# Kernel optimization log

Measured on AMD Instinct MI355X. Metric: run time of the kernel, lower is better.

The kernel has to match this reference:

```python
import jax, jax.numpy as jnp
import numpy as np

H = 16      # num_attention_heads
D = 1024    # hidden_size
DH = D // H # attention_head_size
LN_EPS = 1e-5


def setup_inputs() -> dict:
    key = jax.random.key(0)
    ks = jax.random.split(key, 12)
    B, S = 2, 2048
    s = 0.02
    return {
        "hidden_states": jax.random.normal(ks[0], (B, S, D), jnp.float32),
        "attention_mask": jnp.zeros((B, 1, 1, S), jnp.float32),
        "Wq": jax.random.normal(ks[1], (D, D), jnp.float32) * s,
        "bq": jnp.zeros((D,), jnp.float32),
        "Wk": jax.random.normal(ks[2], (D, D), jnp.float32) * s,
        "bk": jnp.zeros((D,), jnp.float32),
        "Wv": jax.random.normal(ks[3], (D, D), jnp.float32) * s,
        "bv": jnp.zeros((D,), jnp.float32),
        "med_bias": jax.random.normal(ks[4], (H, 1, 1), jnp.float32) * s,
        "Wo": jax.random.normal(ks[5], (D, D), jnp.float32) * s,
        "bo": jnp.zeros((D,), jnp.float32),
        "gamma": jnp.ones((D,), jnp.float32),
        "beta": jnp.zeros((D,), jnp.float32),
    }


def _heads(x):
    # (B,S,D) -> (B,H,S,DH)
    B, S, _ = x.shape
    return x.reshape(B, S, H, DH).transpose(0, 2, 1, 3)


def reference(hidden_states, attention_mask, Wq, bq, Wk, bk, Wv, bv,
              med_bias, Wo, bo, gamma, beta):
    B, S, _ = hidden_states.shape
    q = _heads(hidden_states @ Wq.T + bq)
    k = _heads(hidden_states @ Wk.T + bk)
    v = _heads(hidden_states @ Wv.T + bv)

    scale = 1.0 / jnp.sqrt(jnp.asarray(DH, hidden_states.dtype))
    # scores: (B,H,S,S); per-head medical bias + additive mask
    scores = jnp.einsum('bhqd,bhkd->bhqk', q, k) * scale
    scores = scores + med_bias[None, :, :, :] + attention_mask
    probs = jax.nn.softmax(scores, axis=-1)  # dropout is identity in eval

    ctx = jnp.einsum('bhqk,bhkd->bhqd', probs, v)
    ctx = ctx.transpose(0, 2, 1, 3).reshape(B, S, D)

    attn_out = ctx @ Wo.T + bo
    x = hidden_states + attn_out

    mu = jnp.mean(x, axis=-1, keepdims=True)
    var = jnp.mean(jnp.square(x - mu), axis=-1, keepdims=True)
    return (x - mu) * jax.lax.rsqrt(var + LN_EPS) * gamma + beta
```

## Files before the change

### kernel.cpp

```cpp
#include <hip/hip_runtime.h>
#include <hip/hip_bf16.h>

#define S_LEN 2048
#define NH 16
#define DH 64
#define DMODEL 1024
#define M_TOT 4096
#define LOG2E 1.44269504f

typedef __attribute__((ext_vector_type(8))) short bf16x8;
typedef __attribute__((ext_vector_type(4))) float f32x4;
typedef unsigned short u16;
typedef unsigned short us8 __attribute__((ext_vector_type(8)));

__device__ inline u16 f2bf(float f) {
    union { float f; unsigned u; } c; c.f = f;
    unsigned r = c.u + 0x7fffu + ((c.u >> 16) & 1u);
    return (u16)(r >> 16);
}

__device__ inline void load_lds16(const u16* g, u16* l) {
    __builtin_amdgcn_global_load_lds((const __attribute__((address_space(1))) void*)g,
                                     (__attribute__((address_space(3))) void*)l, 16, 0, 0);
}

__device__ inline us8 pack8(float4 a, float4 b) {
    us8 o;
    o[0] = f2bf(a.x); o[1] = f2bf(a.y); o[2] = f2bf(a.z); o[3] = f2bf(a.w);
    o[4] = f2bf(b.x); o[5] = f2bf(b.y); o[6] = f2bf(b.z); o[7] = f2bf(b.w);
    return o;
}

__global__ __launch_bounds__(256) void conv_bf16(
    const float* __restrict__ src, u16* __restrict__ dst)
{
    const size_t i = ((size_t)blockIdx.x * 256 + threadIdx.x) * 8;
    const float4 a = *(const float4*)(src + i);
    const float4 b = *(const float4*)(src + i + 4);
    *(us8*)(dst + i) = pack8(a, b);
}

__global__ __launch_bounds__(256) void conv4(
    const float* __restrict__ w0, const float* __restrict__ w1,
    const float* __restrict__ w2, const float* __restrict__ w3,
    u16* __restrict__ dst)
{
    const int z = blockIdx.y;
    const float* src = (z == 0) ? w0 : (z == 1) ? w1 : (z == 2) ? w2 : w3;
    const size_t i = ((size_t)blockIdx.x * 256 + threadIdx.x) * 8;
    const float4 a = *(const float4*)(src + i);
    const float4 b = *(const float4*)(src + i + 4);
    *(us8*)(dst + (size_t)z * (DMODEL * DMODEL) + i) = pack8(a, b);
}

__global__ __launch_bounds__(256) void gen_cm(
    const float* __restrict__ mask, float* __restrict__ cm, u16* __restrict__ cmb)
{
    const int i = blockIdx.x * 256 + threadIdx.x;
    const float c = exp2f(mask[i] * LOG2E);
    cm[i] = c;
    cmb[i] = f2bf(c);
}

__global__ __launch_bounds__(256) void gemm_qkv(
    const u16* __restrict__ hsb, const u16* __restrict__ wbf,
    const float* __restrict__ bq, const float* __restrict__ bk, const float* __restrict__ bv,
    const float* __restrict__ cm,
    u16* __restrict__ qb, u16* __restrict__ kb, u16* __restrict__ vT)
{
    __shared__ u16 lA[2][128 * 32];
    __shared__ u16 lB[2][128 * 32];
    const int tid = threadIdx.x, lane = tid & 63, w = tid >> 6;
    const int l15 = lane & 15, lg = lane >> 4;
    const int wr = w >> 1, wc = w & 1;
    const int m0 = blockIdx.y * 128, n0 = blockIdx.x * 128;
    const int z = blockIdx.z;
    const u16* Wp = wbf + (size_t)z * (DMODEL * DMODEL);
    const float* bias = (z == 0) ? bq : (z == 1) ? bk : bv;

    const u16 *aptr[2], *wptr[2]; int adst[2];
#pragma unroll
    for (int i = 0; i < 2; ++i) {
        const int rowb = (w * 2 + i) * 16;
        const int row = rowb + (lane >> 2);
        const int gc = (lane & 3) ^ ((row >> 1) & 3);
        aptr[i] = hsb + (size_t)(m0 + row) * DMODEL + gc * 8;
        wptr[i] = Wp + (size_t)(n0 + row) * DMODEL + gc * 8;
        adst[i] = rowb * 32;
    }
    int afo[4], bfo[4];
#pragma unroll
    for (int i = 0; i < 4; ++i) {
        const int rA = wr * 64 + i * 16 + l15;
        afo[i] = rA * 32 + ((lg ^ ((rA >> 1) & 3)) * 8);
        const int rB = wc * 64 + i * 16 + l15;
        bfo[i] = rB * 32 + ((lg ^ ((rB >> 1) & 3)) * 8);
    }

    f32x4 acc[4][4] = {};

#pragma unroll
    for (int i = 0; i < 2; ++i) {
        load_lds16(aptr[i], &lA[0][adst[i]]);
        load_lds16(wptr[i], &lB[0][adst[i]]);
    }

    int cur = 0;
    for (int t = 0; t < 32; ++t) {
        if (t < 31) {
#pragma unroll
            for (int i = 0; i < 2; ++i) {
                load_lds16(aptr[i] + (t + 1) * 32, &lA[cur ^ 1][adst[i]]);
                load_lds16(wptr[i] + (t + 1) * 32, &lB[cur ^ 1][adst[i]]);
            }
            asm volatile("s_waitcnt vmcnt(4)" ::: "memory");
        } else {
            asm volatile("s_waitcnt vmcnt(0)" ::: "memory");
        }
        __builtin_amdgcn_s_barrier();
        __builtin_amdgcn_sched_barrier(0);

        bf16x8 af[4], bfr[4];
#pragma unroll
        for (int i = 0; i < 4; ++i) {
            af[i] = *(bf16x8*)&lA[cur][afo[i]];
            bfr[i] = *(bf16x8*)&lB[cur][bfo[i]];
        }
        __builtin_amdgcn_s_setprio(1);
#pragma unroll
        for (int i = 0; i < 4; ++i)
#pragma unroll
            for (int j = 0; j < 4; ++j)
                acc[i][j] = __builtin_amdgcn_mfma_f32_16x16x32_bf16(af[i], bfr[j], acc[i][j], 0, 0, 0);
        __builtin_amdgcn_s_setprio(0);
        __builtin_amdgcn_s_barrier();
        cur ^= 1;
    }

    const float qsc = 0.125f * LOG2E;
    float bn[4];
#pragma unroll
    for (int j = 0; j < 4; ++j) bn[j] = bias[n0 + wc * 64 + j * 16 + l15];

#pragma unroll
    for (int i = 0; i < 4; ++i) {
        const int mbase = m0 + wr * 64 + i * 16 + lg * 4;
        if (z == 0) {
#pragma unroll
            for (int j = 0; j < 4; ++j) {
                const int n = n0 + wc * 64 + j * 16 + l15;
#pragma unroll
                for (int e = 0; e < 4; ++e)
                    qb[(size_t)(mbase + e) * DMODEL + n] = f2bf((acc[i][j][e] + bn[j]) * qsc);
            }
        } else if (z == 1) {
#pragma unroll
            for (int j = 0; j < 4; ++j) {
                const int n = n0 + wc * 64 + j * 16 + l15;
#pragma unroll
                for (int e = 0; e < 4; ++e)
                    kb[(size_t)(mbase + e) * DMODEL + n] = f2bf(acc[i][j][e] + bn[j]);
            }
        } else {
            const int bb = mbase >> 11, s = mbase & 2047;
            const float4 c4 = *(const float4*)&cm[bb * S_LEN + s];
#pragma unroll
            for (int j = 0; j < 4; ++j) {
                const int n = n0 + wc * 64 + j * 16 + l15;
                const int hh = n >> 6, dh = n & 63;
                ushort4 uv;
                uv.x = f2bf((acc[i][j][0] + bn[j]) * c4.x);
                uv.y = f2bf((acc[i][j][1] + bn[j]) * c4.y);
                uv.z = f2bf((acc[i][j][2] + bn[j]) * c4.z);
                uv.w = f2bf((acc[i][j][3] + bn[j]) * c4.w);
                *(ushort4*)&vT[((size_t)(bb * NH + hh) * DH + dh) * S_LEN + s] = uv;
            }
        }
    }
}

__global__ __launch_bounds__(256) void gemm_o(
    const u16* __restrict__ ctx, const u16* __restrict__ wobf,
    const float* __restrict__ bo, const float* __restrict__ resid,
    float* __restrict__ X)
{
    __shared__ u16 lA[2][128 * 32];
    __shared__ u16 lB[2][128 * 32];
    const int tid = threadIdx.x, lane = tid & 63, w = tid >> 6;
    const int l15 = lane & 15, lg = lane >> 4;
    const int wr = w >> 1, wc = w & 1;
    const int m0 = blockIdx.y * 128, n0 = blockIdx.x * 128;

    const u16 *aptr[2], *wptr[2]; int adst[2];
#pragma unroll
    for (int i = 0; i < 2; ++i) {
        const int rowb = (w * 2 + i) * 16;
        const int row = rowb + (lane >> 2);
        const int gc = (lane & 3) ^ ((row >> 1) & 3);
        aptr[i] = ctx + (size_t)(m0 + row) * DMODEL + gc * 8;
        wptr[i] = wobf + (size_t)(n0 + row) * DMODEL + gc * 8;
        adst[i] = rowb * 32;
    }
    int afo[4], bfo[4];
#pragma unroll
    for (int i = 0; i < 4; ++i) {
        const int rA = wr * 64 + i * 16 + l15;
        afo[i] = rA * 32 + ((lg ^ ((rA >> 1) & 3)) * 8);
        const int rB = wc * 64 + i * 16 + l15;
        bfo[i] = rB * 32 + ((lg ^ ((rB >> 1) & 3)) * 8);
    }

    f32x4 acc[4][4] = {};

#pragma unroll
    for (int i = 0; i < 2; ++i) {
        load_lds16(aptr[i], &lA[0][adst[i]]);
        load_lds16(wptr[i], &lB[0][adst[i]]);
    }

    int cur = 0;
    for (int t = 0; t < 32; ++t) {
        if (t < 31) {
#pragma unroll
            for (int i = 0; i < 2; ++i) {
                load_lds16(aptr[i] + (t + 1) * 32, &lA[cur ^ 1][adst[i]]);
                load_lds16(wptr[i] + (t + 1) * 32, &lB[cur ^ 1][adst[i]]);
            }
            asm volatile("s_waitcnt vmcnt(4)" ::: "memory");
        } else {
            asm volatile("s_waitcnt vmcnt(0)" ::: "memory");
        }
        __builtin_amdgcn_s_barrier();
        __builtin_amdgcn_sched_barrier(0);

        bf16x8 af[4], bfr[4];
#pragma unroll
        for (int i = 0; i < 4; ++i) {
            af[i] = *(bf16x8*)&lA[cur][afo[i]];
            bfr[i] = *(bf16x8*)&lB[cur][bfo[i]];
        }
        __builtin_amdgcn_s_setprio(1);
#pragma unroll
        for (int i = 0; i < 4; ++i)
#pragma unroll
            for (int j = 0; j < 4; ++j)
                acc[i][j] = __builtin_amdgcn_mfma_f32_16x16x32_bf16(af[i], bfr[j], acc[i][j], 0, 0, 0);
        __builtin_amdgcn_s_setprio(0);
        __builtin_amdgcn_s_barrier();
        cur ^= 1;
    }

#pragma unroll
    for (int i = 0; i < 4; ++i) {
#pragma unroll
        for (int j = 0; j < 4; ++j) {
            const int n = n0 + wc * 64 + j * 16 + l15;
            const float bnj = bo[n];
#pragma unroll
            for (int e = 0; e < 4; ++e) {
                const int m = m0 + wr * 64 + i * 16 + lg * 4 + e;
                X[(size_t)m * DMODEL + n] = acc[i][j][e] + bnj + resid[(size_t)m * DMODEL + n];
            }
        }
    }
}

__global__ __launch_bounds__(512, 4) void attn9(
    const u16* __restrict__ qg, const u16* __restrict__ kg,
    const u16* __restrict__ vTg, const u16* __restrict__ cmb,
    u16* __restrict__ ctx)
{
    __shared__ u16 Kl[2][128 * 64];
    __shared__ u16 Vl[2][64 * 128];
    __shared__ u16 Pl8[8][16 * 64];

    const int tid = threadIdx.x, lane = tid & 63, w = tid >> 6;
    const int bx = blockIdx.x;
    const int x = bx & 7, rest = bx >> 3;
    const int qt = rest & 15, g2 = rest >> 4;
    const int hb = g2 * 8 + x;
    const int h = hb & (NH - 1), b = hb >> 4;

    const int l15 = lane & 15, lg = lane >> 4;
    const int q0 = qt * 128 + w * 16;
    const size_t rowbase = (size_t)b * S_LEN * DMODEL + h * DH;
    const size_t vbase = (size_t)(b * NH + h) * DH * S_LEN;
    u16* Pw = Pl8[w];

    bf16x8 aq[2];
#pragma unroll
    for (int kf = 0; kf < 2; ++kf)
        aq[kf] = *(const bf16x8*)&qg[rowbase + (size_t)(q0 + l15) * DMODEL + kf * 32 + lg * 8];

    const int lx = l15 & 7;
    int kbase[2];
#pragma unroll
    for (int kf = 0; kf < 2; ++kf)
        kbase[kf] = l15 * 64 + (((kf * 4 + lg) ^ lx) * 8);
    int vb2[4];
#pragma unroll
    for (int kf2 = 0; kf2 < 4; ++kf2)
        vb2[kf2] = l15 * 128 + (((kf2 * 4 + lg) ^ lx) * 8);
    const int phi = l15 >> 3, plo = l15 & 7;

    size_t ksoff[2], vsoff[2];
    int ldst[2];
#pragma unroll
    for (int t = 0; t < 2; ++t) {
        const int ck = t * 512 + tid;
        const int krow = ck >> 3, kslot = ck & 7;
        ksoff[t] = (size_t)krow * DMODEL + ((kslot ^ (krow & 7)) * 8);
        const int vrow = ck >> 4, vslot = ck & 15;
        vsoff[t] = (size_t)vrow * S_LEN + ((vslot ^ (vrow & 7)) * 8);
        ldst[t] = (t * 512 + w * 64) * 8;
    }
    const u16* cmb_b = cmb + (size_t)b * S_LEN + lg * 8;

    f32x4 po[4] = {};
    f32x4 pol = {};

    bf16x8 cf[4];
#pragma unroll
    for (int j = 0; j < 4; ++j)
        cf[j] = *(const bf16x8*)&cmb_b[j * 32];
    const u16* kp = kg + rowbase;
    const u16* vp = vTg + vbase;
#pragma unroll
    for (int t = 0; t < 2; ++t) {
        load_lds16(kp + ksoff[t], &Kl[0][ldst[t]]);
        load_lds16(vp + vsoff[t], &Vl[0][ldst[t]]);
    }
    kp += 128 * DMODEL; vp += 128;

    int cur = 0;
    for (int kt = 0; kt < S_LEN / 128; ++kt) {
        bf16x8 nx[4];
        if (kt + 1 < S_LEN / 128) {
#pragma unroll
            for (int j = 0; j < 4; ++j)
                nx[j] = *(const bf16x8*)&cmb_b[(kt + 1) * 128 + j * 32];
#pragma unroll
            for (int t = 0; t < 2; ++t) {
                load_lds16(kp + ksoff[t], &Kl[cur ^ 1][ldst[t]]);
                load_lds16(vp + vsoff[t], &Vl[cur ^ 1][ldst[t]]);
            }
            kp += 128 * DMODEL; vp += 128;
            asm volatile("s_waitcnt vmcnt(8)" ::: "memory");
        } else {
#pragma unroll
            for (int j = 0; j < 4; ++j) nx[j] = cf[j];
            asm volatile("s_waitcnt vmcnt(0)" ::: "memory");
        }
        __builtin_amdgcn_s_barrier();
        __builtin_amdgcn_sched_barrier(0);

#pragma unroll
        for (int h2 = 0; h2 < 2; ++h2) {
            f32x4 sa[4] = {};
            bf16x8 bkf[4][2];
#pragma unroll
            for (int nf = 0; nf < 4; ++nf)
#pragma unroll
                for (int kf = 0; kf < 2; ++kf)
                    bkf[nf][kf] = *(bf16x8*)&Kl[cur][(h2 * 4 + nf) * 1024 + kbase[kf]];
            __builtin_amdgcn_s_setprio(1);
#pragma unroll
            for (int nf = 0; nf < 4; ++nf)
#pragma unroll
                for (int kf = 0; kf < 2; ++kf)
                    sa[nf] = __builtin_amdgcn_mfma_f32_16x16x32_bf16(aq[kf], bkf[nf][kf], sa[nf], 0, 0, 0);
            __builtin_amdgcn_s_setprio(0);

#pragma unroll
            for (int e = 0; e < 4; ++e) {
                const int prow = lg * 4 + e;
                const int pbase = prow * 64 + plo;
                const int pxor = prow & 7;
#pragma unroll
                for (int nf = 0; nf < 4; ++nf) {
                    union { float f; unsigned u; } cv;
                    cv.f = exp2f(sa[nf][e]);
                    Pw[pbase + (((nf * 2 + phi) ^ pxor) * 8)] = (u16)(cv.u >> 16);
                }
            }

#pragma unroll
            for (int j = 0; j < 2; ++j) {
                const int kf2 = h2 * 2 + j;
                bf16x8 ap = *(bf16x8*)&Pw[kbase[j]];
                bf16x8 bv[4];
#pragma unroll
                for (int df = 0; df < 4; ++df)
                    bv[df] = *(bf16x8*)&Vl[cur][df * 2048 + vb2[kf2]];
                const bf16x8 cfk = cf[kf2];
                __builtin_amdgcn_s_setprio(1);
#pragma unroll
                for (int df = 0; df < 4; ++df)
                    po[df] = __builtin_amdgcn_mfma_f32_16x16x32_bf16(ap, bv[df], po[df], 0, 0, 0);
                pol = __builtin_amdgcn_mfma_f32_16x16x32_bf16(ap, cfk, pol, 0, 0, 0);
                __builtin_amdgcn_s_setprio(0);
            }
        }
        __builtin_amdgcn_s_barrier();
#pragma unroll
        for (int j = 0; j < 4; ++j) cf[j] = nx[j];
        cur ^= 1;
    }

#pragma unroll
    for (int e = 0; e < 4; ++e) {
        const float inv = 1.0f / pol[e];
        const int qrow = q0 + lg * 4 + e;
#pragma unroll
        for (int df = 0; df < 4; ++df)
            ctx[((size_t)b * S_LEN + qrow) * DMODEL + h * DH + df * 16 + l15] = f2bf(po[df][e] * inv);
    }
}

__global__ __launch_bounds__(256) void ln_kernel(
    const float* __restrict__ xin, float* __restrict__ y,
    const float* __restrict__ gamma, const float* __restrict__ beta)
{
    const int row = blockIdx.x;
    const int tid = threadIdx.x;
    float4 vv = *(const float4*)(xin + (size_t)row * DMODEL + tid * 4);
    float s = vv.x + vv.y + vv.z + vv.w;
    float s2 = vv.x * vv.x + vv.y * vv.y + vv.z * vv.z + vv.w * vv.w;
#pragma unroll
    for (int d = 1; d < 64; d <<= 1) { s += __shfl_xor(s, d); s2 += __shfl_xor(s2, d); }
    __shared__ float rs[4], rs2[4];
    if ((tid & 63) == 0) { rs[tid >> 6] = s; rs2[tid >> 6] = s2; }
    __syncthreads();
    s = rs[0] + rs[1] + rs[2] + rs[3];
    s2 = rs2[0] + rs2[1] + rs2[2] + rs2[3];
    const float mu = s * (1.f / DMODEL);
    const float var = s2 * (1.f / DMODEL) - mu * mu;
    const float inv = rsqrtf(var + 1e-5f);
    const float4 g = *(const float4*)(gamma + tid * 4);
    const float4 bt = *(const float4*)(beta + tid * 4);
    vv.x = (vv.x - mu) * inv * g.x + bt.x;
    vv.y = (vv.y - mu) * inv * g.y + bt.y;
    vv.z = (vv.z - mu) * inv * g.z + bt.z;
    vv.w = (vv.w - mu) * inv * g.w + bt.w;
    *(float4*)(y + (size_t)row * DMODEL + tid * 4) = vv;
}

extern "C" void kernel_launch(void* const* d_in, const int* in_sizes, int n_in,
                              void* d_out, int out_size, void* d_ws, size_t ws_size,
                              hipStream_t stream) {
    const float* hs    = (const float*)d_in[0];
    const float* mask  = (const float*)d_in[1];
    const float* Wq    = (const float*)d_in[2];
    const float* bq    = (const float*)d_in[3];
    const float* Wk    = (const float*)d_in[4];
    const float* bk    = (const float*)d_in[5];
    const float* Wv    = (const float*)d_in[6];
    const float* bv    = (const float*)d_in[7];
    const float* Wo    = (const float*)d_in[9];
    const float* bo    = (const float*)d_in[10];
    const float* gamma = (const float*)d_in[11];
    const float* beta  = (const float*)d_in[12];
    float* out = (float*)d_out;

    const size_t MN = (size_t)M_TOT * DMODEL;
    const size_t WN = (size_t)DMODEL * DMODEL;
    u16* qb      = (u16*)d_ws;
    u16* kb      = qb + MN;
    u16* vT      = kb + MN;
    u16* scratch = vT + MN;
    float* X     = (float*)d_ws;

    u16*  wbf = (u16*)out;
    float* cm = out + MN - 4096 - 2048;
    u16*  cmb = (u16*)(out + MN - 2048);

    dim3 blk(256);

    conv_bf16<<<MN / 2048, blk, 0, stream>>>(hs, scratch);
    conv4<<<dim3(WN / 2048, 4), blk, 0, stream>>>(Wq, Wk, Wv, Wo, wbf);
    gen_cm<<<(2 * S_LEN) / 256, blk, 0, stream>>>(mask, cm, cmb);
    gemm_qkv<<<dim3(DMODEL / 128, M_TOT / 128, 3), blk, 0, stream>>>(
        scratch, wbf, bq, bk, bv, cm, qb, kb, vT);
    attn9<<<dim3(512), dim3(512), 0, stream>>>(qb, kb, vT, cmb, scratch);
    gemm_o<<<dim3(DMODEL / 128, M_TOT / 128), blk, 0, stream>>>(
        scratch, wbf + 3 * WN, bo, hs, X);
    ln_kernel<<<M_TOT, blk, 0, stream>>>(X, out, gamma, beta);
}
```

Measured before the change: 152.9 us.

## Merge prep kernels, remap GEMM blocks per XCD, use raw v_exp in softmax

Folds the three conversion kernels (hidden-state bf16 cast, weight casts, mask exp) into one launch to save launch overhead. Remaps the QKV and output-projection GEMM block indices so each XCD handles a contiguous tile region, aiming for better L2 reuse across chiplets. Swaps exp2f for a raw v_exp_f32 inline asm in the attention softmax to avoid the range-handling code around the library call. The raw exp loses denormal/edge handling, and the volatile asm with s_nop may limit instruction scheduling.

```diff
diff --git a/kernel.cpp b/kernel.cpp
--- a/kernel.cpp
+++ b/kernel.cpp
@@ -19,6 +19,12 @@
     return (u16)(r >> 16);
 }
 
+__device__ inline float exp2_raw(float x) {
+    float r;
+    asm volatile("v_exp_f32 %0, %1\n\ts_nop 0" : "=v"(r) : "v"(x));
+    return r;
+}
+
 __device__ inline void load_lds16(const u16* g, u16* l) {
     __builtin_amdgcn_global_load_lds((const __attribute__((address_space(1))) void*)g,
                                      (__attribute__((address_space(3))) void*)l, 16, 0, 0);
@@ -31,35 +37,33 @@
     return o;
 }
 
-__global__ __launch_bounds__(256) void conv_bf16(
-    const float* __restrict__ src, u16* __restrict__ dst)
-{
-    const size_t i = ((size_t)blockIdx.x * 256 + threadIdx.x) * 8;
-    const float4 a = *(const float4*)(src + i);
-    const float4 b = *(const float4*)(src + i + 4);
-    *(us8*)(dst + i) = pack8(a, b);
-}
-
-__global__ __launch_bounds__(256) void conv4(
+__global__ __launch_bounds__(256) void prep(
+    const float* __restrict__ hs,
     const float* __restrict__ w0, const float* __restrict__ w1,
     const float* __restrict__ w2, const float* __restrict__ w3,
-    u16* __restrict__ dst)
+    const float* __restrict__ mask,
+    u16* __restrict__ hsb, u16* __restrict__ wbf,
+    float* __restrict__ cm, u16* __restrict__ cmb)
 {
-    const int z = blockIdx.y;
-    const float* src = (z == 0) ? w0 : (z == 1) ? w1 : (z == 2) ? w2 : w3;
-    const size_t i = ((size_t)blockIdx.x * 256 + threadIdx.x) * 8;
-    const float4 a = *(const float4*)(src + i);
-    const float4 b = *(const float4*)(src + i + 4);
-    *(us8*)(dst + (size_t)z * (DMODEL * DMODEL) + i) = pack8(a, b);
-}
-
-__global__ __launch_bounds__(256) void gen_cm(
-    const float* __restrict__ mask, float* __restrict__ cm, u16* __restrict__ cmb)
-{
-    const int i = blockIdx.x * 256 + threadIdx.x;
-    const float c = exp2f(mask[i] * LOG2E);
-    cm[i] = c;
-    cmb[i] = f2bf(c);
+    const int bid = blockIdx.x;
+    if (bid < 2048) {
+        const size_t i = ((size_t)bid * 256 + threadIdx.x) * 8;
+        const float4 a = *(const float4*)(hs + i);
+        const float4 b = *(const float4*)(hs + i + 4);
+        *(us8*)(hsb + i) = pack8(a, b);
+    } else if (bid < 4096) {
+        const int z = (bid - 2048) >> 9;
+        const float* src = (z == 0) ? w0 : (z == 1) ? w1 : (z == 2) ? w2 : w3;
+        const size_t i = ((size_t)((bid - 2048) & 511) * 256 + threadIdx.x) * 8;
+        const float4 a = *(const float4*)(src + i);
+        const float4 b = *(const float4*)(src + i + 4);
+        *(us8*)(wbf + (size_t)z * (DMODEL * DMODEL) + i) = pack8(a, b);
+    } else {
+        const int i = (bid - 4096) * 256 + threadIdx.x;
+        const float c = exp2_raw(mask[i] * LOG2E);
+        cm[i] = c;
+        cmb[i] = f2bf(c);
+    }
 }
 
 __global__ __launch_bounds__(256) void gemm_qkv(
@@ -73,8 +77,13 @@
     const int tid = threadIdx.x, lane = tid & 63, w = tid >> 6;
     const int l15 = lane & 15, lg = lane >> 4;
     const int wr = w >> 1, wc = w & 1;
-    const int m0 = blockIdx.y * 128, n0 = blockIdx.x * 128;
-    const int z = blockIdx.z;
+
+    const int flat = blockIdx.x + 8 * (blockIdx.y + 32 * blockIdx.z);
+    const int xcd = flat & 7, l = flat >> 3;
+    const int z = l >> 5, r = l & 31;
+    const int n0 = ((xcd >> 2) * 4 + (r >> 3)) * 128;
+    const int m0 = ((xcd & 3) * 8 + (r & 7)) * 128;
+
     const u16* Wp = wbf + (size_t)z * (DMODEL * DMODEL);
     const float* bias = (z == 0) ? bq : (z == 1) ? bk : bv;
 
@@ -189,7 +198,11 @@
     const int tid = threadIdx.x, lane = tid & 63, w = tid >> 6;
     const int l15 = lane & 15, lg = lane >> 4;
     const int wr = w >> 1, wc = w & 1;
-    const int m0 = blockIdx.y * 128, n0 = blockIdx.x * 128;
+
+    const int flat = blockIdx.x + 8 * blockIdx.y;
+    const int xcd = flat & 7, l = flat >> 3;
+    const int n0 = ((xcd >> 2) * 4 + (l >> 3)) * 128;
+    const int m0 = ((xcd & 3) * 8 + (l & 7)) * 128;
 
     const u16 *aptr[2], *wptr[2]; int adst[2];
 #pragma unroll
@@ -265,7 +278,7 @@
     }
 }
 
-__global__ __launch_bounds__(512, 4) void attn9(
+__global__ __launch_bounds__(512, 4) void attn11(
     const u16* __restrict__ qg, const u16* __restrict__ kg,
     const u16* __restrict__ vTg, const u16* __restrict__ cmb,
     u16* __restrict__ ctx)
@@ -379,7 +392,7 @@
 #pragma unroll
                 for (int nf = 0; nf < 4; ++nf) {
                     union { float f; unsigned u; } cv;
-                    cv.f = exp2f(sa[nf][e]);
+                    cv.f = exp2_raw(sa[nf][e]);
                     Pw[pbase + (((nf * 2 + phi) ^ pxor) * 8)] = (u16)(cv.u >> 16);
                 }
             }
@@ -476,13 +489,12 @@
 
     dim3 blk(256);
 
-    conv_bf16<<<MN / 2048, blk, 0, stream>>>(hs, scratch);
-    conv4<<<dim3(WN / 2048, 4), blk, 0, stream>>>(Wq, Wk, Wv, Wo, wbf);
-    gen_cm<<<(2 * S_LEN) / 256, blk, 0, stream>>>(mask, cm, cmb);
-    gemm_qkv<<<dim3(DMODEL / 128, M_TOT / 128, 3), blk, 0, stream>>>(
+    prep<<<dim3(4112), blk, 0, stream>>>(hs, Wq, Wk, Wv, Wo, mask,
+                                         scratch, wbf, cm, cmb);
+    gemm_qkv<<<dim3(8, 32, 3), blk, 0, stream>>>(
         scratch, wbf, bq, bk, bv, cm, qb, kb, vT);
-    attn9<<<dim3(512), dim3(512), 0, stream>>>(qb, kb, vT, cmb, scratch);
-    gemm_o<<<dim3(DMODEL / 128, M_TOT / 128), blk, 0, stream>>>(
+    attn11<<<dim3(512), dim3(512), 0, stream>>>(qb, kb, vT, cmb, scratch);
+    gemm_o<<<dim3(8, 32), blk, 0, stream>>>(
         scratch, wbf + 3 * WN, bo, hs, X);
     ln_kernel<<<M_TOT, blk, 0, stream>>>(X, out, gamma, beta);
 }
```

Result: faster. 143.0 us, median of 2 (-6.5%).
